# Optimization experiments

Hardware: AMD Instinct MI355X
Metric: run time of the kernel (lower is better)

## Reference

```python
import jax, jax.numpy as jnp
import numpy as np

N_IMG = 512
N_ANGLES = 180


def _bilinear(img, sy, sx):
    """Bilinear sample img at float coords (sy, sx); zero outside the image."""
    n = img.shape[0]
    y0 = jnp.floor(sy)
    x0 = jnp.floor(sx)
    wy = sy - y0
    wx = sx - x0
    y0i = y0.astype(jnp.int32)
    x0i = x0.astype(jnp.int32)

    def gather(yi, xi):
        valid = (yi >= 0) & (yi < n) & (xi >= 0) & (xi < n)
        yc = jnp.clip(yi, 0, n - 1)
        xc = jnp.clip(xi, 0, n - 1)
        return jnp.where(valid, img[yc, xc], jnp.zeros((), img.dtype))

    v00 = gather(y0i, x0i)
    v01 = gather(y0i, x0i + 1)
    v10 = gather(y0i + 1, x0i)
    v11 = gather(y0i + 1, x0i + 1)
    return (v00 * (1 - wy) * (1 - wx) + v01 * (1 - wy) * wx
            + v10 * wy * (1 - wx) + v11 * wy * wx)


def _radon(img, angles):
    """skimage-style radon: rotate image by each angle, sum along axis 0.
    Returns sinogram of shape (n_detectors, n_angles) = (N, len(angles))."""
    n = img.shape[0]
    c = (n - 1) * 0.5  # rotation about image center
    coords = jnp.arange(n, dtype=img.dtype) - c
    yc, xc = jnp.meshgrid(coords, coords, indexing="ij")  # (N, N)

    def one_angle(theta_deg):
        t = jnp.deg2rad(theta_deg.astype(img.dtype))
        co, si = jnp.cos(t), jnp.sin(t)
        # inverse-rotation sampling coordinates (CCW rotation of the image)
        sx = co * xc + si * yc + c
        sy = -si * xc + co * yc + c
        rotated = _bilinear(img, sy, sx)  # (N, N)
        return rotated.sum(axis=0)        # projection along detector rows -> (N,)

    sino = jax.vmap(one_angle)(angles)  # (n_angles, N)
    return sino.T                        # (N, n_angles)


def setup_inputs() -> dict:
    key = jax.random.key(0)
    img = jax.random.uniform(key, (N_IMG, N_IMG), dtype=jnp.float32)  # nonnegative PET activity
    angles = jnp.arange(N_ANGLES, dtype=jnp.int32)  # degrees 0..179 (skimage default)
    return {"img": img, "angles": angles}


def reference(img, angles):
    return _radon(img, angles)
```

## Files before the change

kernel.cpp:

```cpp
#include <hip/hip_runtime.h>
#include <hip/hip_fp16.h>
#include <stdint.h>

#define N 512
#define NA 180
#define TD 64
#define TI 64
#define TW 100
#define TH 94
#define TILE_DW (37 * 256)
#define PP 708
#define PR 704
#define POFF 96

#define WS_IMGPB  0
#define WS_IMGTPB (PR * PP)
#define WS_TAB    (2 * PR * PP)
#define WS_FLAGS  (WS_TAB + 4 * NA)
#define WS_OUTT   997888

__device__ __forceinline__ void load16_to_lds(const uint32_t* g, uint32_t* l) {
    __builtin_amdgcn_global_load_lds(
        (const __attribute__((address_space(1))) void*)g,
        (__attribute__((address_space(3))) void*)l,
        16 , 0 , 0 );
}

__global__ __launch_bounds__(256) void pad_kernel(const float* __restrict__ img,
                                                  const int* __restrict__ angles,
                                                  uint32_t* __restrict__ imgPB,
                                                  uint32_t* __restrict__ imgTPB,
                                                  float4* __restrict__ tab,
                                                  int* __restrict__ flags,
                                                  float* __restrict__ outT) {
    __shared__ float lds[65 * 66];
    const int lane = threadIdx.x & 63;
    const int wq   = threadIdx.x >> 6;
    const int bx = blockIdx.x, by = blockIdx.y;
    const int b  = by * 11 + bx;

    if (b < 90) {
        float4 z; z.x = z.y = z.z = z.w = 0.0f;
        ((float4*)outT)[b * 256 + threadIdx.x] = z;
    }
    if (b == 120 && threadIdx.x < NA) {
        float t = (float)angles[threadIdx.x] * 0.017453292519943295f;
        float si = sinf(t), co = cosf(t);
        int useT = fabsf(si) > fabsf(co);
        float4 e;
        if (useT) { e.x = co; e.y = -si; e.z = si; e.w = co; }
        else      { e.x = si; e.y = co;  e.z = co; e.w = -si; }
        tab[threadIdx.x] = e;
        flags[threadIdx.x] = useT;
    }

    for (int idx = threadIdx.x; idx < 65 * 65; idx += 256) {
        int r = idx / 65, cc = idx - r * 65;
        int y = by * 64 + r - POFF, x = bx * 64 + cc - POFF;
        bool in = ((unsigned)y < N) && ((unsigned)x < N);
        lds[r * 66 + cc] = in ? img[y * N + x] : 0.0f;
    }
    __syncthreads();
#pragma unroll
    for (int j = 0; j < 16; ++j) {
        int r = wq * 16 + j;
        float v0 = lds[r * 66 + lane], v1 = lds[r * 66 + lane + 1];
        __half2 h = __halves2half2(__float2half(v0), __float2half(v1));
        imgPB[(size_t)(by * 64 + r) * PP + bx * 64 + lane] = *(uint32_t*)&h;
        float t0 = lds[lane * 66 + r], t1 = lds[(lane + 1) * 66 + r];
        __half2 ht = __halves2half2(__float2half(t0), __float2half(t1));
        imgTPB[(size_t)(bx * 64 + r) * PP + by * 64 + lane] = *(uint32_t*)&ht;
    }
}

__global__ __launch_bounds__(256, 4) void radon_kernel(const uint32_t* __restrict__ imgPB,
                                                       const uint32_t* __restrict__ imgTPB,
                                                       const float4* __restrict__ tab,
                                                       const int* __restrict__ flags,
                                                       float* __restrict__ outT) {
    __shared__ uint32_t tile[TILE_DW];

    const int tid  = threadIdx.x;
    const int lane = tid & 63;
    const int wave = tid >> 6;
    const int d0 = blockIdx.x * TD;
    const int a  = blockIdx.y;
    const int i0 = blockIdx.z * TI;

    const float c = 255.5f;
    const float4 tb = tab[a];
    const float au = tb.x, bus = tb.y, av = tb.z, bvs = tb.w;

    const float fi0 = (float)i0 - c, fi1 = (float)(i0 + TI - 1) - c;
    const float xc0 = (float)d0 - c, xc1 = (float)(d0 + TD - 1) - c;
    const float buA = fmaf(bus, xc0, c), buB = fmaf(bus, xc1, c);
    const float bvA = fmaf(bvs, xc0, c), bvB = fmaf(bvs, xc1, c);
    const float buMin = fminf(buA, buB), buMax = fmaxf(buA, buB);
    const float bvMin = fminf(bvA, bvB), bvMax = fmaxf(bvA, bvB);
    const float fiLoU = (au >= 0.0f) ? fi0 : fi1, fiHiU = (au >= 0.0f) ? fi1 : fi0;
    const float fiLoV = (av >= 0.0f) ? fi0 : fi1, fiHiV = (av >= 0.0f) ? fi1 : fi0;
    const float umin = fmaf(au, fiLoU, buMin), umax = fmaf(au, fiHiU, buMax);
    const float vmin = fmaf(av, fiLoV, bvMin), vmax = fmaf(av, fiHiV, bvMax);

    if (umin > (float)N || umax < -1.0f || vmin > (float)N || vmax < -1.0f) return;

    const int ub0 = (((int)floorf(umin)) & ~3) - 4;
    const int vb  = ((int)floorf(vmin)) - 1;

    const uint32_t* __restrict__ src = flags[a] ? imgTPB : imgPB;
    const uint32_t* gbase = src + (vb + POFF) * PP + (ub0 + POFF);

#pragma unroll
    for (int s = 0; s < 10; ++s) {
        int chunk = s * 4 + wave;
        if (chunk < 37) {
            int tt = chunk * 256 + (lane << 2);
            int r  = tt / TW;
            int cc = tt - r * TW;
            load16_to_lds(gbase + r * PP + cc, &tile[chunk * 256]);
        }
    }
    __syncthreads();

    const float xcl = (float)(d0 + lane) - c;
    const float bu_l2 = fmaf(bus, xcl, c) - (float)ub0;
    const float bv_l2 = fmaf(bvs, xcl, c) - (float)vb;

    float s1 = 0.0f, s2 = 0.0f;
    float fi = (float)(i0 + wave * 16) - c;
#pragma unroll
    for (int k = 0; k < 16; ++k) {
        float u = fmaf(au, fi, bu_l2);
        float v = fmaf(av, fi, bv_l2);
        fi += 1.0f;
        float x0 = floorf(u), y0 = floorf(v);
        float wx = u - x0, wy = v - y0;
        float af = fmaf(y0, (float)TW, x0);
        int ai = (int)af;
        uint32_t P0 = tile[ai];
        uint32_t P1 = tile[ai + TW];
        __half2 p0h = *(__half2*)&P0;
        __half2 p1h = *(__half2*)&P1;
        __half2 dv  = __hsub2(p1h, p0h);
        __half2 wy2 = __float2half2_rn(wy);
        __half2 m   = __hfma2(wy2, dv, p0h);
        float lf = __low2float(m), hf = __high2float(m);
        s2 = fmaf(wx, hf - lf, s2);
        s1 += lf;
    }

    __syncthreads();
    float* ft = (float*)tile;
    ft[tid] = s1 + s2;
    __syncthreads();
    if (tid < 64) {
        float r = ft[tid] + ft[tid + 64] + ft[tid + 128] + ft[tid + 192];
        atomicAdd(&outT[a * 512 + d0 + tid], r);
    }
}

__global__ __launch_bounds__(256) void txo_kernel(const float* __restrict__ outT,
                                                  float* __restrict__ out) {
    __shared__ float lds[64 * 65];
    const int lane = threadIdx.x & 63;
    const int wq   = threadIdx.x >> 6;
    const int d0 = blockIdx.x * 64;
    const int a0 = blockIdx.y * 64;
#pragma unroll
    for (int j = 0; j < 16; ++j) {
        int r = wq * 16 + j;
        int a = a0 + r;
        lds[r * 65 + lane] = (a < NA) ? outT[a * 512 + d0 + lane] : 0.0f;
    }
    __syncthreads();
#pragma unroll
    for (int j = 0; j < 16; ++j) {
        int r = wq * 16 + j;
        int aa = a0 + lane;
        if (aa < NA) out[(d0 + r) * NA + aa] = lds[lane * 65 + r];
    }
}

extern "C" void kernel_launch(void* const* d_in, const int* in_sizes, int n_in,
                              void* d_out, int out_size, void* d_ws, size_t ws_size,
                              hipStream_t stream) {
    const float* img  = (const float*)d_in[0];
    const int* angles = (const int*)d_in[1];
    float* out = (float*)d_out;
    float* ws  = (float*)d_ws;

    uint32_t* imgPB  = (uint32_t*)(ws + WS_IMGPB);
    uint32_t* imgTPB = (uint32_t*)(ws + WS_IMGTPB);
    float4*   tab    = (float4*)(ws + WS_TAB);
    int*      flags  = (int*)(ws + WS_FLAGS);
    float*    outT   = ws + WS_OUTT;

    dim3 pgrid(11, 11);
    pad_kernel<<<pgrid, 256, 0, stream>>>(img, angles, imgPB, imgTPB, tab, flags, outT);

    dim3 grid(N / TD, NA, N / TI);
    radon_kernel<<<grid, 256, 0, stream>>>(imgPB, imgTPB, tab, flags, outT);

    dim3 tgrid(512 / 64, 3);
    txo_kernel<<<tgrid, 256, 0, stream>>>(outT, out);
}
```

Baseline: 103.3 us.

## Use 512-thread radon blocks, narrower LDS tile, and fdot2 bilinear interpolation

Doubles the radon block to 512 threads (8 waves, each doing 8 rows instead of 16) so more waves per block share the same LDS tile load. It also shrinks the tile width to 96 dwords by aligning ub0 more tightly. The inner loop now uses fract, packed RTZ conversion and a packed-half fdot2 for the horizontal lerp. This cuts per-thread ALU work and the number of tile bytes loaded per block. In exchange it puts more pressure on the block-level reduction and relies on the tighter tile bounds staying in range, and rounding changes from RN to RTZ.

```diff
diff --git a/kernel.cpp b/kernel.cpp
--- a/kernel.cpp
+++ b/kernel.cpp
@@ -6,9 +6,8 @@
 #define NA 180
 #define TD 64
 #define TI 64
-#define TW 100
-#define TH 94
-#define TILE_DW (37 * 256)
+#define TW 96
+#define TILE_DW (36 * 256)
 #define PP 708
 #define PR 704
 #define POFF 96
@@ -18,6 +17,13 @@
 #define WS_TAB    (2 * PR * PP)
 #define WS_FLAGS  (WS_TAB + 4 * NA)
 #define WS_OUTT   997888
+
+typedef _Float16 hh2 __attribute__((ext_vector_type(2)));
+union H2U { uint32_t u; hh2 h; };
+
+__device__ __forceinline__ hh2 cvt_pkrtz(float a, float b) {
+    return __builtin_bit_cast(hh2, __builtin_amdgcn_cvt_pkrtz(a, b));
+}
 
 __device__ __forceinline__ void load16_to_lds(const uint32_t* g, uint32_t* l) {
     __builtin_amdgcn_global_load_lds(
@@ -73,7 +79,7 @@
     }
 }
 
-__global__ __launch_bounds__(256, 4) void radon_kernel(const uint32_t* __restrict__ imgPB,
+__global__ __launch_bounds__(512, 8) void radon_kernel(const uint32_t* __restrict__ imgPB,
                                                        const uint32_t* __restrict__ imgTPB,
                                                        const float4* __restrict__ tab,
                                                        const int* __restrict__ flags,
@@ -104,16 +110,16 @@
 
     if (umin > (float)N || umax < -1.0f || vmin > (float)N || vmax < -1.0f) return;
 
-    const int ub0 = (((int)floorf(umin)) & ~3) - 4;
+    const int ub0 = (((int)floorf(umin)) - 1) & ~3;
     const int vb  = ((int)floorf(vmin)) - 1;
 
     const uint32_t* __restrict__ src = flags[a] ? imgTPB : imgPB;
     const uint32_t* gbase = src + (vb + POFF) * PP + (ub0 + POFF);
 
 #pragma unroll
-    for (int s = 0; s < 10; ++s) {
-        int chunk = s * 4 + wave;
-        if (chunk < 37) {
+    for (int s = 0; s < 5; ++s) {
+        int chunk = s * 8 + wave;
+        if (chunk < 36) {
             int tt = chunk * 256 + (lane << 2);
             int r  = tt / TW;
             int cc = tt - r * TW;
@@ -123,38 +129,40 @@
     __syncthreads();
 
     const float xcl = (float)(d0 + lane) - c;
-    const float bu_l2 = fmaf(bus, xcl, c) - (float)ub0;
-    const float bv_l2 = fmaf(bvs, xcl, c) - (float)vb;
-
-    float s1 = 0.0f, s2 = 0.0f;
-    float fi = (float)(i0 + wave * 16) - c;
-#pragma unroll
-    for (int k = 0; k < 16; ++k) {
-        float u = fmaf(au, fi, bu_l2);
-        float v = fmaf(av, fi, bv_l2);
+    const float buL = fmaf(bus, xcl, c) - (float)ub0;
+    const float bvL = fmaf(bvs, xcl, c) - (float)vb;
+
+    float s = 0.0f;
+    float fi = (float)(i0 + wave * 8) - c;
+#pragma unroll
+    for (int k = 0; k < 8; ++k) {
+        float u = fmaf(au, fi, buL);
+        float v = fmaf(av, fi, bvL);
         fi += 1.0f;
-        float x0 = floorf(u), y0 = floorf(v);
-        float wx = u - x0, wy = v - y0;
-        float af = fmaf(y0, (float)TW, x0);
-        int ai = (int)af;
-        uint32_t P0 = tile[ai];
-        uint32_t P1 = tile[ai + TW];
-        __half2 p0h = *(__half2*)&P0;
-        __half2 p1h = *(__half2*)&P1;
-        __half2 dv  = __hsub2(p1h, p0h);
-        __half2 wy2 = __float2half2_rn(wy);
-        __half2 m   = __hfma2(wy2, dv, p0h);
-        float lf = __low2float(m), hf = __high2float(m);
-        s2 = fmaf(wx, hf - lf, s2);
-        s1 += lf;
+        float wx = __builtin_amdgcn_fractf(u);
+        float wy = __builtin_amdgcn_fractf(v);
+        int iu = (int)u, iv = (int)v;
+        int ai = iv * TW + iu;
+        H2U P0, P1;
+        P0.u = tile[ai];
+        P1.u = tile[ai + TW];
+        hh2 wy2 = cvt_pkrtz(wy, wy);
+        hh2 m   = wy2 * (P1.h - P0.h) + P0.h;
+        hh2 wv  = cvt_pkrtz(1.0f - wx, wx);
+#if __has_builtin(__builtin_amdgcn_fdot2)
+        s = __builtin_amdgcn_fdot2(wv, m, s, false);
+#else
+        s += (1.0f - wx) * (float)m.x + wx * (float)m.y;
+#endif
     }
 
     __syncthreads();
     float* ft = (float*)tile;
-    ft[tid] = s1 + s2;
+    ft[tid] = s;
     __syncthreads();
     if (tid < 64) {
-        float r = ft[tid] + ft[tid + 64] + ft[tid + 128] + ft[tid + 192];
+        float r = ft[tid]       + ft[tid + 64]  + ft[tid + 128] + ft[tid + 192]
+                + ft[tid + 256] + ft[tid + 320] + ft[tid + 384] + ft[tid + 448];
         atomicAdd(&outT[a * 512 + d0 + tid], r);
     }
 }
@@ -199,7 +207,7 @@
     pad_kernel<<<pgrid, 256, 0, stream>>>(img, angles, imgPB, imgTPB, tab, flags, outT);
 
     dim3 grid(N / TD, NA, N / TI);
-    radon_kernel<<<grid, 256, 0, stream>>>(imgPB, imgTPB, tab, flags, outT);
+    radon_kernel<<<grid, 512, 0, stream>>>(imgPB, imgTPB, tab, flags, outT);
 
     dim3 tgrid(512 / 64, 3);
     txo_kernel<<<tgrid, 256, 0, stream>>>(outT, out);
```

Measured after the change: 100.6 us. -2.6%, faster.
